# Kernel tuning notes

Measured on AMD Instinct MI355X. Metric: run time of the kernel, lower is better.

Reference implementation:

```python
import jax, jax.numpy as jnp
import numpy as np


def _reflect(x, size):
    # PyTorch grid_sample reflection padding, align_corners=False:
    # reflect about borders at -0.5 and size-0.5, then clip to [0, size-1].
    x = x + 0.5
    x = jnp.mod(x, 2.0 * size)
    x = jnp.where(x >= size, 2.0 * size - x, x)
    x = x - 0.5
    return jnp.clip(x, 0.0, size - 1.0)


def _grid_sample_one(img, grid):
    # img: (H, W, C); grid: (H, W, 2) with (x, y) in [-1, 1]
    H, W, _ = img.shape
    # unnormalize, align_corners=False
    ix = ((grid[..., 0] + 1.0) * W - 1.0) * 0.5
    iy = ((grid[..., 1] + 1.0) * H - 1.0) * 0.5
    ix = _reflect(ix, W)
    iy = _reflect(iy, H)
    x0 = jnp.floor(ix)
    y0 = jnp.floor(iy)
    wx = (ix - x0)[..., None]
    wy = (iy - y0)[..., None]
    x0i = jnp.clip(x0, 0, W - 1).astype(jnp.int32)
    x1i = jnp.clip(x0 + 1.0, 0, W - 1).astype(jnp.int32)
    y0i = jnp.clip(y0, 0, H - 1).astype(jnp.int32)
    y1i = jnp.clip(y0 + 1.0, 0, H - 1).astype(jnp.int32)
    Ia = img[y0i, x0i]  # (H, W, C)
    Ib = img[y0i, x1i]
    Ic = img[y1i, x0i]
    Id = img[y1i, x1i]
    return (Ia * (1 - wx) * (1 - wy) + Ib * wx * (1 - wy)
            + Ic * (1 - wx) * wy + Id * wx * wy)


def _displace(image, displacement_map, amplitude, angle):
    N, H, W, C = image.shape
    # base sampling grid, torch.linspace(-1, 1, size) endpoints included
    gy, gx = jnp.meshgrid(jnp.linspace(-1.0, 1.0, H, dtype=image.dtype),
                          jnp.linspace(-1.0, 1.0, W, dtype=image.dtype),
                          indexing='ij')
    base = jnp.stack([gx, gy], axis=-1)  # (H, W, 2) as (x, y)
    # bilinear resize (half-pixel centers == torch align_corners=False)
    dm = jax.image.resize(displacement_map,
                          (N, H, W, displacement_map.shape[-1]),
                          method='bilinear')
    if dm.shape[-1] == 3:
        dm = jnp.mean(dm, axis=-1)  # (N, H, W)
    else:
        dm = dm[..., 0]
    d = dm * amplitude[:, None, None]
    dx = jnp.cos(angle)[:, None, None] * d / (W - 1) * 2.0
    dy = jnp.sin(angle)[:, None, None] * d / (H - 1) * 2.0
    grid = base[None] + jnp.stack([dx, dy], axis=-1)  # (N, H, W, 2)
    return jax.vmap(_grid_sample_one)(image, grid)  # (N, H, W, C)


def setup_inputs() -> dict:
    key = jax.random.key(0)
    k1, k2, k3, k4 = jax.random.split(key, 4)
    N, H, W, C = 8, 1024, 1024, 3
    image = jax.random.normal(k1, (N, H, W, C), dtype=jnp.float32)
    displacement_map = jax.random.uniform(k2, (N, 512, 512, 3), dtype=jnp.float32)
    amplitude = jax.random.uniform(k3, (N,), dtype=jnp.float32) * 20.0  # pixels
    angle = jax.random.uniform(k4, (N,), dtype=jnp.float32) * 2.0 * np.pi
    return {"image": image, "displacement_map": displacement_map,
            "amplitude": amplitude, "angle": angle}


def reference(image, displacement_map, amplitude, angle):
    return _displace(image, displacement_map, amplitude, angle)
```

## Files before the change

kernel.cpp:

```cpp
#include <hip/hip_runtime.h>
#include <math.h>
#include <limits.h>

typedef float f4u __attribute__((ext_vector_type(4), aligned(4)));
typedef float f2u __attribute__((ext_vector_type(2), aligned(4)));

__device__ __forceinline__ float reflect_pre(float xr, float size, float two, float inv_two) {
    xr = xr - floorf(xr * inv_two) * two;
    if (xr >= size) xr = two - xr;
    xr -= 0.5f;
    return fminf(fmaxf(xr, 0.0f), size - 1.0f);
}

__global__ __launch_bounds__(256, 4) void displace_tile_kernel(
    const float* __restrict__ img,
    const float* __restrict__ dmap,
    const float* __restrict__ amp,
    const float* __restrict__ ang,
    float* __restrict__ out,
    int N, int H, int W, int DH, int DW,
    int tiles_x, int tiles_per_img, unsigned nb)
{
    unsigned id  = blockIdx.x;
    unsigned q   = nb >> 3, r = nb & 7u;
    unsigned xcd = id & 7u, off = id >> 3;
    unsigned orig = (xcd < r) ? (xcd * (q + 1u) + off)
                              : (r * (q + 1u) + (xcd - r) * q + off);

    int n    = (int)(orig / (unsigned)tiles_per_img);
    int rem  = (int)(orig % (unsigned)tiles_per_img);
    int ty_t = rem / tiles_x;
    int tx_t = rem % tiles_x;

    int lane = (int)(threadIdx.x & 63u);
    int warp = (int)(threadIdx.x >> 6u);

    int w  = tx_t * 64 + lane;
    int h0 = ty_t * 16 + warp * 4;

    int M  = h0 >> 1;
    int fx = (w >> 1) - 1 + (w & 1);
    float tx = (w & 1) ? 0.25f : 0.75f;
    int qd = min(max(fx, 0), DW - 2);
    bool hiA = (fx >= DW - 1);
    bool loB = (fx < 0);

    const float* dbase = dmap + (long long)n * DH * DW * 3;
    f4u dv[4]; f2u du[4];
    #pragma unroll
    for (int j = 0; j < 4; ++j) {
        int rj = min(max(M - 1 + j, 0), DH - 1);
        const float* pr = dbase + ((long long)rj * DW + qd) * 3;
        dv[j] = *(const f4u*)pr;
        du[j] = *(const f2u*)(pr + 4);
    }

    float a = amp[n];
    float sa, ca;
    sincosf(ang[n], &sa, &ca);
    float cW = (float)W / (float)(W - 1);
    float cH = (float)H / (float)(H - 1);
    float kxc = ca * a * cW;
    float kyc = sa * a * cH;
    float twoW = 2.0f * (float)W, twoH = 2.0f * (float)H;
    float invTwoW = 1.0f / twoW, invTwoH = 1.0f / twoH;
    const float s3 = 1.0f / 3.0f;

    float Rr[4];
    #pragma unroll
    for (int j = 0; j < 4; ++j) {
        float mlo = dv[j].x + dv[j].y + dv[j].z;
        float mhi = dv[j].w + du[j].x + du[j].y;
        float A = hiA ? mhi : mlo;
        float B = loB ? mlo : mhi;
        Rr[j] = A + tx * (B - A);
    }

    float wxv[4], wyv[4];
    const float* PA[4];
    const float* PB[4];
    bool  CL[4];
    const float* ibase = img + (long long)n * H * W * 3;

    const int   jlo[4] = {0, 1, 1, 2};
    const float tyv[4] = {0.75f, 0.25f, 0.75f, 0.25f};

    #pragma unroll
    for (int p = 0; p < 4; ++p) {
        float Ra = Rr[jlo[p]], Rb = Rr[jlo[p] + 1];
        float dm = (Ra + tyv[p] * (Rb - Ra)) * s3;

        float rx = (float)w * cW        + dm * kxc;
        float ry = (float)(h0 + p) * cH + dm * kyc;
        float ix = reflect_pre(rx, (float)W, twoW, invTwoW);
        float iy = reflect_pre(ry, (float)H, twoH, invTwoH);

        float x0f = floorf(ix), y0f = floorf(iy);
        wxv[p] = ix - x0f;
        wyv[p] = iy - y0f;
        int ix0 = (int)x0f;
        int jy0 = (int)y0f;
        int jy1 = min(jy0 + 1, H - 1);
        int qx  = min(ix0, W - 2);
        CL[p] = (ix0 > qx);
        PA[p] = ibase + ((long long)jy0 * W + qx) * 3;
        PB[p] = ibase + ((long long)jy1 * W + qx) * 3;
    }

    f4u va[4], vb[4]; f2u ua[4], ub[4];
    #pragma unroll
    for (int p = 0; p < 4; ++p) {
        va[p] = *(const f4u*)PA[p];
        ua[p] = *(const f2u*)(PA[p] + 4);
        vb[p] = *(const f4u*)PB[p];
        ub[p] = *(const f2u*)(PB[p] + 4);
    }
    __builtin_amdgcn_sched_barrier(0);

    long long obase = ((long long)(n * H + h0) * W + w) * 3;
    #pragma unroll
    for (int p = 0; p < 4; ++p) {
        float wx = wxv[p], wy = wyv[p];
        float wa = (1.0f - wx) * (1.0f - wy);
        float wb = wx * (1.0f - wy);
        float wc = (1.0f - wx) * wy;
        float wd = wx * wy;
        bool cl = CL[p];

        float A0 = cl ? va[p].w : va[p].x, A1 = cl ? ua[p].x : va[p].y, A2 = cl ? ua[p].y : va[p].z;
        float B0 = va[p].w,                B1 = ua[p].x,                B2 = ua[p].y;
        float C0 = cl ? vb[p].w : vb[p].x, C1 = cl ? ub[p].x : vb[p].y, C2 = cl ? ub[p].y : vb[p].z;
        float D0 = vb[p].w,                D1 = ub[p].x,                D2 = ub[p].y;

        float* o = out + obase + (long long)p * W * 3;
        o[0] = A0 * wa + B0 * wb + C0 * wc + D0 * wd;
        o[1] = A1 * wa + B1 * wb + C1 * wc + D1 * wd;
        o[2] = A2 * wa + B2 * wb + C2 * wc + D2 * wd;
    }
}

__device__ __forceinline__ float reflect_coord(float x, float size) {
    x += 0.5f;
    float two = 2.0f * size;
    x = x - floorf(x / two) * two;
    if (x >= size) x = two - x;
    x -= 0.5f;
    return fminf(fmaxf(x, 0.0f), size - 1.0f);
}

__global__ __launch_bounds__(256) void displace_kernel(
    const float* __restrict__ img, const float* __restrict__ dmap,
    const float* __restrict__ amp, const float* __restrict__ ang,
    float* __restrict__ out, int N, int H, int W, int DH, int DW)
{
    long long idx = (long long)blockIdx.x * blockDim.x + threadIdx.x;
    long long total = (long long)N * H * W;
    if (idx >= total) return;
    int w = (int)(idx % W);
    long long t = idx / W;
    int h = (int)(t % H);
    int n = (int)(t / H);

    float sx = (w + 0.5f) * ((float)DW / (float)W) - 0.5f;
    float sy = (h + 0.5f) * ((float)DH / (float)H) - 0.5f;
    float fx = floorf(sx), fy = floorf(sy);
    float tx = sx - fx, ty = sy - fy;
    int dx0 = max(0, min(DW - 1, (int)fx));
    int dx1 = max(0, min(DW - 1, (int)fx + 1));
    int dy0 = max(0, min(DH - 1, (int)fy));
    int dy1 = max(0, min(DH - 1, (int)fy + 1));

    const float* dbase = dmap + (long long)n * DH * DW * 3;
    const float* p00 = dbase + ((long long)dy0 * DW + dx0) * 3;
    const float* p01 = dbase + ((long long)dy0 * DW + dx1) * 3;
    const float* p10 = dbase + ((long long)dy1 * DW + dx0) * 3;
    const float* p11 = dbase + ((long long)dy1 * DW + dx1) * 3;
    float m00 = p00[0] + p00[1] + p00[2];
    float m01 = p01[0] + p01[1] + p01[2];
    float m10 = p10[0] + p10[1] + p10[2];
    float m11 = p11[0] + p11[1] + p11[2];
    float dmv = ((m00 * (1.0f - tx) + m01 * tx) * (1.0f - ty)
               + (m10 * (1.0f - tx) + m11 * tx) * ty) * (1.0f / 3.0f);

    float a = amp[n];
    float sa, ca;
    sincosf(ang[n], &sa, &ca);
    float d = dmv * a;
    float ddx = ca * d * (2.0f / (float)(W - 1));
    float ddy = sa * d * (2.0f / (float)(H - 1));
    float gx = -1.0f + 2.0f * (float)w / (float)(W - 1) + ddx;
    float gy = -1.0f + 2.0f * (float)h / (float)(H - 1) + ddy;
    float ix = ((gx + 1.0f) * (float)W - 1.0f) * 0.5f;
    float iy = ((gy + 1.0f) * (float)H - 1.0f) * 0.5f;
    ix = reflect_coord(ix, (float)W);
    iy = reflect_coord(iy, (float)H);

    float x0f = floorf(ix), y0f = floorf(iy);
    float wx = ix - x0f, wy = iy - y0f;
    int ix0 = min((int)x0f, W - 1);
    int ix1 = min((int)x0f + 1, W - 1);
    int iy0 = min((int)y0f, H - 1);
    int iy1 = min((int)y0f + 1, H - 1);

    const float* ibase = img + (long long)n * H * W * 3;
    const float* Ia = ibase + ((long long)iy0 * W + ix0) * 3;
    const float* Ib = ibase + ((long long)iy0 * W + ix1) * 3;
    const float* Ic = ibase + ((long long)iy1 * W + ix0) * 3;
    const float* Id = ibase + ((long long)iy1 * W + ix1) * 3;
    float wa = (1.0f - wx) * (1.0f - wy);
    float wb = wx * (1.0f - wy);
    float wc = (1.0f - wx) * wy;
    float wd = wx * wy;
    float* o = out + idx * 3;
    #pragma unroll
    for (int c = 0; c < 3; ++c)
        o[c] = Ia[c] * wa + Ib[c] * wb + Ic[c] * wc + Id[c] * wd;
}

extern "C" void kernel_launch(void* const* d_in, const int* in_sizes, int n_in,
                              void* d_out, int out_size, void* d_ws, size_t ws_size,
                              hipStream_t stream) {
    const float* img  = (const float*)d_in[0];
    const float* dmap = (const float*)d_in[1];
    const float* amp  = (const float*)d_in[2];
    const float* ang  = (const float*)d_in[3];
    float* out = (float*)d_out;

    int N = in_sizes[2];
    long long hw  = (long long)in_sizes[0] / ((long long)N * 3);
    int H = (int)llround(sqrt((double)hw));
    int W = H;
    long long dhw = (long long)in_sizes[1] / ((long long)N * 3);
    int DH = (int)llround(sqrt((double)dhw));
    int DW = DH;

    bool fast = (W % 64 == 0) && (H % 16 == 0) && (W == 2 * DW) && (H == 2 * DH) &&
                (DW >= 2) && ((long long)H * W <= (long long)INT_MAX);

    if (fast) {
        int tiles_x = W / 64;
        int tiles_y = H / 16;
        int tpi = tiles_x * tiles_y;
        unsigned nb = (unsigned)((long long)tpi * N);
        displace_tile_kernel<<<nb, 256, 0, stream>>>(
            img, dmap, amp, ang, out, N, H, W, DH, DW, tiles_x, tpi, nb);
    } else {
        long long total = (long long)N * H * W;
        int block = 256;
        long long grid = (total + block - 1) / block;
        displace_kernel<<<(dim3)(unsigned)grid, block, 0, stream>>>(
            img, dmap, amp, ang, out, N, H, W, DH, DW);
    }
}
```

Before: 208.9 us.

## Stage per-tile image band in shared memory before bilinear gathers

Each block computes a conservative bounding box of source pixels its 64x16 tile can reference, given the maximum displacement and reflection. If the box fits, it copies that band cooperatively from global memory into LDS with vector loads, then performs the four-tap gathers from LDS. Otherwise it falls back to the direct global gather. This trades redundant scattered global/L2 gathers for a coalesced band load plus a barrier and about 40KB of LDS per block, which may cut occupancy under launch_bounds(256,4).

```diff
diff --git a/kernel.cpp b/kernel.cpp
--- a/kernel.cpp
+++ b/kernel.cpp
@@ -4,12 +4,36 @@
 
 typedef float f4u __attribute__((ext_vector_type(4), aligned(4)));
 typedef float f2u __attribute__((ext_vector_type(2), aligned(4)));
+
+#define TILE_W 64
+#define TILE_H 16
+#define XB 88
+#define YB 38
+#define XBF (XB * 3)
 
 __device__ __forceinline__ float reflect_pre(float xr, float size, float two, float inv_two) {
     xr = xr - floorf(xr * inv_two) * two;
     if (xr >= size) xr = two - xr;
     xr -= 0.5f;
     return fminf(fmaxf(xr, 0.0f), size - 1.0f);
+}
+
+__device__ __forceinline__ void px_taps(int w, int h, float dm,
+    float cW, float cH, float kxc, float kyc, int W, int H,
+    float twoW, float twoH, float invTwoW, float invTwoH,
+    int& qx, int& jy0, int& jy1, float& wx, float& wy, bool& cl)
+{
+    float rx = (float)w * cW + dm * kxc;
+    float ry = (float)h * cH + dm * kyc;
+    float ix = reflect_pre(rx, (float)W, twoW, invTwoW);
+    float iy = reflect_pre(ry, (float)H, twoH, invTwoH);
+    float x0f = floorf(ix), y0f = floorf(iy);
+    wx = ix - x0f;  wy = iy - y0f;
+    int ix0 = (int)x0f;
+    jy0 = (int)y0f;
+    jy1 = min(jy0 + 1, H - 1);
+    qx  = min(ix0, W - 2);
+    cl  = (ix0 > qx);
 }
 
 __global__ __launch_bounds__(256, 4) void displace_tile_kernel(
@@ -21,6 +45,8 @@
     int N, int H, int W, int DH, int DW,
     int tiles_x, int tiles_per_img, unsigned nb)
 {
+    __shared__ __align__(16) float band[YB * XBF];
+
     unsigned id  = blockIdx.x;
     unsigned q   = nb >> 3, r = nb & 7u;
     unsigned xcd = id & 7u, off = id >> 3;
@@ -35,12 +61,14 @@
     int lane = (int)(threadIdx.x & 63u);
     int warp = (int)(threadIdx.x >> 6u);
 
-    int w  = tx_t * 64 + lane;
-    int h0 = ty_t * 16 + warp * 4;
+    int x0 = tx_t * TILE_W;
+    int hT = ty_t * TILE_H;
+    int w  = x0 + lane;
+    int h0 = hT + warp * 4;
 
     int M  = h0 >> 1;
     int fx = (w >> 1) - 1 + (w & 1);
-    float tx = (w & 1) ? 0.25f : 0.75f;
+    float txd = (w & 1) ? 0.25f : 0.75f;
     int qd = min(max(fx, 0), DW - 2);
     bool hiA = (fx >= DW - 1);
     bool loB = (fx < 0);
@@ -66,6 +94,30 @@
     float invTwoW = 1.0f / twoW, invTwoH = 1.0f / twoH;
     const float s3 = 1.0f / 3.0f;
 
+    float ixmin = (float)x0 * cW - 0.5f + fminf(0.0f, kxc);
+    float ixmax = (float)(x0 + TILE_W - 1) * cW - 0.5f + fmaxf(0.0f, kxc);
+    float iymin = (float)hT * cH - 0.5f + fminf(0.0f, kyc);
+    float iymax = (float)(hT + TILE_H - 1) * cH - 0.5f + fmaxf(0.0f, kyc);
+
+    int xlo = (int)floorf(ixmin);
+    int xhi = (int)floorf(ixmax) + 1;
+    if (ixmin < -0.5f)            xhi = max(xhi, (int)floorf(-ixmin - 1.0f) + 1);
+    if (ixmax > (float)W - 0.5f)  xlo = min(xlo, (int)floorf(twoW - ixmax - 1.0f));
+    xlo = max(0, xlo);  xhi = min(W - 1, xhi);
+
+    int ylo = (int)floorf(iymin);
+    int yhi = (int)floorf(iymax) + 1;
+    if (iymin < -0.5f)            yhi = max(yhi, (int)floorf(-iymin - 1.0f) + 1);
+    if (iymax > (float)H - 0.5f)  ylo = min(ylo, (int)floorf(twoH - iymax - 1.0f));
+    ylo = max(0, ylo);  yhi = min(H - 1, yhi);
+
+    int cols  = xhi - xlo + 1;
+    int colsp = (cols + 3) & ~3;
+    int rowsn = yhi - ylo + 1;
+    bool ok = (colsp <= XB) && (rowsn <= YB) && (colsp <= W);
+
+    const float* ibase = img + (long long)n * H * W * 3;
+
     float Rr[4];
     #pragma unroll
     for (int j = 0; j < 4; ++j) {
@@ -73,69 +125,96 @@
         float mhi = dv[j].w + du[j].x + du[j].y;
         float A = hiA ? mhi : mlo;
         float B = loB ? mlo : mhi;
-        Rr[j] = A + tx * (B - A);
+        Rr[j] = A + txd * (B - A);
     }
-
-    float wxv[4], wyv[4];
-    const float* PA[4];
-    const float* PB[4];
-    bool  CL[4];
-    const float* ibase = img + (long long)n * H * W * 3;
-
     const int   jlo[4] = {0, 1, 1, 2};
     const float tyv[4] = {0.75f, 0.25f, 0.75f, 0.25f};
 
-    #pragma unroll
-    for (int p = 0; p < 4; ++p) {
-        float Ra = Rr[jlo[p]], Rb = Rr[jlo[p] + 1];
-        float dm = (Ra + tyv[p] * (Rb - Ra)) * s3;
-
-        float rx = (float)w * cW        + dm * kxc;
-        float ry = (float)(h0 + p) * cH + dm * kyc;
-        float ix = reflect_pre(rx, (float)W, twoW, invTwoW);
-        float iy = reflect_pre(ry, (float)H, twoH, invTwoH);
-
-        float x0f = floorf(ix), y0f = floorf(iy);
-        wxv[p] = ix - x0f;
-        wyv[p] = iy - y0f;
-        int ix0 = (int)x0f;
-        int jy0 = (int)y0f;
-        int jy1 = min(jy0 + 1, H - 1);
-        int qx  = min(ix0, W - 2);
-        CL[p] = (ix0 > qx);
-        PA[p] = ibase + ((long long)jy0 * W + qx) * 3;
-        PB[p] = ibase + ((long long)jy1 * W + qx) * 3;
-    }
-
-    f4u va[4], vb[4]; f2u ua[4], ub[4];
-    #pragma unroll
-    for (int p = 0; p < 4; ++p) {
-        va[p] = *(const f4u*)PA[p];
-        ua[p] = *(const f2u*)(PA[p] + 4);
-        vb[p] = *(const f4u*)PB[p];
-        ub[p] = *(const f2u*)(PB[p] + 4);
-    }
-    __builtin_amdgcn_sched_barrier(0);
-
     long long obase = ((long long)(n * H + h0) * W + w) * 3;
-    #pragma unroll
-    for (int p = 0; p < 4; ++p) {
-        float wx = wxv[p], wy = wyv[p];
-        float wa = (1.0f - wx) * (1.0f - wy);
-        float wb = wx * (1.0f - wy);
-        float wc = (1.0f - wx) * wy;
-        float wd = wx * wy;
-        bool cl = CL[p];
-
-        float A0 = cl ? va[p].w : va[p].x, A1 = cl ? ua[p].x : va[p].y, A2 = cl ? ua[p].y : va[p].z;
-        float B0 = va[p].w,                B1 = ua[p].x,                B2 = ua[p].y;
-        float C0 = cl ? vb[p].w : vb[p].x, C1 = cl ? ub[p].x : vb[p].y, C2 = cl ? ub[p].y : vb[p].z;
-        float D0 = vb[p].w,                D1 = ub[p].x,                D2 = ub[p].y;
-
-        float* o = out + obase + (long long)p * W * 3;
-        o[0] = A0 * wa + B0 * wb + C0 * wc + D0 * wd;
-        o[1] = A1 * wa + B1 * wb + C1 * wc + D1 * wd;
-        o[2] = A2 * wa + B2 * wb + C2 * wc + D2 * wd;
+
+    if (ok) {
+        xlo = min(xlo, W - colsp);
+
+        int chunks = (colsp * 3) >> 2;
+        for (int row = warp; row < rowsn; row += 4) {
+            const float* g = ibase + ((long long)(ylo + row) * W + xlo) * 3;
+            float* l = band + row * XBF;
+            for (int c = lane; c < chunks; c += 64) {
+                f4u v = *(const f4u*)(g + 4 * c);
+                float4 t; t.x = v.x; t.y = v.y; t.z = v.z; t.w = v.w;
+                *(float4*)(l + 4 * c) = t;
+            }
+        }
+        __syncthreads();
+
+        int b0[4], b1[4]; float wxv[4], wyv[4]; bool CL[4];
+        #pragma unroll
+        for (int p = 0; p < 4; ++p) {
+            float Ra = Rr[jlo[p]], Rb = Rr[jlo[p] + 1];
+            float dm = (Ra + tyv[p] * (Rb - Ra)) * s3;
+            int qx, jy0, jy1; float wx, wy; bool cl;
+            px_taps(w, h0 + p, dm, cW, cH, kxc, kyc, W, H,
+                    twoW, twoH, invTwoW, invTwoH, qx, jy0, jy1, wx, wy, cl);
+            int ldx = min(max(qx - xlo, 0), colsp - 2);
+            int ly0 = min(max(jy0 - ylo, 0), rowsn - 1);
+            int ly1 = min(max(jy1 - ylo, 0), rowsn - 1);
+            b0[p] = ly0 * XBF + ldx * 3;
+            b1[p] = ly1 * XBF + ldx * 3;
+            wxv[p] = wx; wyv[p] = wy; CL[p] = cl;
+        }
+
+        float t0[4][6], t1[4][6];
+        #pragma unroll
+        for (int p = 0; p < 4; ++p) {
+            #pragma unroll
+            for (int j = 0; j < 6; ++j) {
+                t0[p][j] = band[b0[p] + j];
+                t1[p][j] = band[b1[p] + j];
+            }
+        }
+
+        #pragma unroll
+        for (int p = 0; p < 4; ++p) {
+            float wx = wxv[p], wy = wyv[p];
+            float wa = (1.0f - wx) * (1.0f - wy);
+            float wb = wx * (1.0f - wy);
+            float wc = (1.0f - wx) * wy;
+            float wd = wx * wy;
+            bool cl = CL[p];
+            float A0 = cl ? t0[p][3] : t0[p][0], A1 = cl ? t0[p][4] : t0[p][1], A2 = cl ? t0[p][5] : t0[p][2];
+            float B0 = t0[p][3],                 B1 = t0[p][4],                 B2 = t0[p][5];
+            float C0 = cl ? t1[p][3] : t1[p][0], C1 = cl ? t1[p][4] : t1[p][1], C2 = cl ? t1[p][5] : t1[p][2];
+            float D0 = t1[p][3],                 D1 = t1[p][4],                 D2 = t1[p][5];
+            float* o = out + obase + (long long)p * W * 3;
+            o[0] = A0 * wa + B0 * wb + C0 * wc + D0 * wd;
+            o[1] = A1 * wa + B1 * wb + C1 * wc + D1 * wd;
+            o[2] = A2 * wa + B2 * wb + C2 * wc + D2 * wd;
+        }
+    } else {
+        #pragma unroll
+        for (int p = 0; p < 4; ++p) {
+            float Ra = Rr[jlo[p]], Rb = Rr[jlo[p] + 1];
+            float dm = (Ra + tyv[p] * (Rb - Ra)) * s3;
+            int qx, jy0, jy1; float wx, wy; bool cl;
+            px_taps(w, h0 + p, dm, cW, cH, kxc, kyc, W, H,
+                    twoW, twoH, invTwoW, invTwoH, qx, jy0, jy1, wx, wy, cl);
+            const float* PA = ibase + ((long long)jy0 * W + qx) * 3;
+            const float* PB = ibase + ((long long)jy1 * W + qx) * 3;
+            f4u va = *(const f4u*)PA;  f2u ua = *(const f2u*)(PA + 4);
+            f4u vb = *(const f4u*)PB;  f2u ub = *(const f2u*)(PB + 4);
+            float wa = (1.0f - wx) * (1.0f - wy);
+            float wb = wx * (1.0f - wy);
+            float wc = (1.0f - wx) * wy;
+            float wd = wx * wy;
+            float A0 = cl ? va.w : va.x, A1 = cl ? ua.x : va.y, A2 = cl ? ua.y : va.z;
+            float B0 = va.w,             B1 = ua.x,             B2 = ua.y;
+            float C0 = cl ? vb.w : vb.x, C1 = cl ? ub.x : vb.y, C2 = cl ? ub.y : vb.z;
+            float D0 = vb.w,             D1 = ub.x,             D2 = ub.y;
+            float* o = out + obase + (long long)p * W * 3;
+            o[0] = A0 * wa + B0 * wb + C0 * wc + D0 * wd;
+            o[1] = A1 * wa + B1 * wb + C1 * wc + D1 * wd;
+            o[2] = A2 * wa + B2 * wb + C2 * wc + D2 * wd;
+        }
     }
 }
 
```

Result: slower. 225.7 us (+8.1%).
